# Kernel optimization log

Hardware: AMD Instinct MI355X
Metric: run time of the kernel (lower is better)

## Reference

```python
import jax, jax.numpy as jnp
import numpy as np

NMS_THRESH = 0.3  # default nms_thresh in DetNet.predict


def setup_inputs() -> dict:
    key = jax.random.key(0)
    k1, k2, k3, k4 = jax.random.split(key, 4)
    W, N = 8, 1024
    det = jax.random.uniform(k1, (W, N, 5), dtype=jnp.float32)          # (conf, cx, cy, w, h) in [0,1)
    offsets = jax.random.uniform(k2, (W, 5), dtype=jnp.float32) * 0.5   # window offset vector (0, left, top, 0, 0)-like
    scales = jax.random.uniform(k3, (W, 5), dtype=jnp.float32) * 0.5 + 0.25  # window scale vector
    b = jax.random.uniform(k4, (W, 4), dtype=jnp.float32)
    # (valid_left, valid_right, valid_top, valid_bottom) with left<right, top<bottom
    bounds = jnp.stack([0.3 * b[:, 0], 0.7 + 0.3 * b[:, 1],
                        0.3 * b[:, 2], 0.7 + 0.3 * b[:, 3]], axis=-1)
    return {"det": det, "offsets": offsets, "scales": scales, "bounds": bounds}


def _pairwise_iou(boxes):
    # boxes: [M,4] in (x1,y1,x2,y2)
    x1, y1, x2, y2 = boxes[:, 0], boxes[:, 1], boxes[:, 2], boxes[:, 3]
    area = jnp.clip(x2 - x1, 0.0) * jnp.clip(y2 - y1, 0.0)              # [M]
    iw = jnp.clip(jnp.minimum(x2[:, None], x2[None, :]) - jnp.maximum(x1[:, None], x1[None, :]), 0.0)
    ih = jnp.clip(jnp.minimum(y2[:, None], y2[None, :]) - jnp.maximum(y1[:, None], y1[None, :]), 0.0)
    inter = iw * ih                                                     # [M,M]
    union = area[:, None] + area[None, :] - inter
    return inter / jnp.maximum(union, 1e-9)


def reference(det, offsets, scales, bounds):
    W, N, _ = det.shape
    M = W * N
    cx, cy = det[..., 1], det[..., 2]                                    # [W,N]
    left, right = bounds[:, 0:1], bounds[:, 1:2]
    top, bottom = bounds[:, 2:3], bounds[:, 3:4]
    valid = (cx < right) & (cx > left) & (cy < bottom) & (cy > top)      # [W,N] border mask
    # torch.addcmul(offset, d, scale) = offset + d * scale
    d = (offsets[:, None, :] + det * scales[:, None, :]).reshape(M, 5)
    valid = valid.reshape(M)
    scores = jnp.where(valid, d[:, 0], -1.0)                             # invalid boxes never kept
    order = jnp.argsort(-scores)                                         # descending confidence
    d_s = d[order]                                                       # [M,5]
    s_s = scores[order]
    # point_form: (cx,cy,w,h) -> (x1,y1,x2,y2)
    cxy, wh = d_s[:, 1:3], d_s[:, 3:5]
    boxes = jnp.concatenate([cxy - wh * 0.5, cxy + wh * 0.5], axis=-1)
    iou = jax.lax.stop_gradient(_pairwise_iou(boxes))                    # [M,M], suppression is non-diff
    s_c = jax.lax.stop_gradient(s_s)
    idx = jnp.arange(M)

    def body(i, keep):
        # suppressed if any kept higher-score box overlaps > thresh
        sup = jnp.any(keep & (idx < i) & (iou[:, i] > NMS_THRESH))
        return keep.at[i].set(jnp.logical_and(~sup, s_c[i] > 0.0))

    keep = jax.lax.fori_loop(0, M, body, jnp.ones((M,), dtype=bool))
    return d_s * keep[:, None].astype(d_s.dtype)                         # [M,5], suppressed rows zeroed
```

## Files before the change

### kernel.cpp

```cpp
#include <hip/hip_runtime.h>
#include <cstdint>


#define M_TOT 8192
#define NMS_T 0.3f

#define WS_BOX   65536
#define WS_D     196608
#define WS_VCNT  360448
#define WS_ZROW  393216
#define WS_DONE  458752
#define WS_MASK  524288

typedef unsigned long long u64t;

__device__ __forceinline__ uint32_t desc_key(float sv) {
    uint32_t u = __float_as_uint(sv);
    uint32_t m = (u & 0x80000000u) ? ~u : (u | 0x80000000u);
    return ~m;
}
__device__ __forceinline__ u64t rdl64(u64t v, int sl) {
    unsigned lo = (unsigned)__builtin_amdgcn_readlane((int)(unsigned)v, sl);
    unsigned hi = (unsigned)__builtin_amdgcn_readlane((int)(unsigned)(v >> 32), sl);
    return ((u64t)hi << 32) | lo;
}

__device__ __forceinline__ void scatter_one(
    int i, int rank, u64t key,
    const float* __restrict__ det, const float* __restrict__ offsets,
    const float* __restrict__ scales,
    float4* __restrict__ boxes_srt, float* __restrict__ d_srt)
{
    uint32_t dkey = (uint32_t)(key >> 16);
    if (dkey >= 0x7FFFFFFFu) return;
    int g = i >> 10;
    float d0 = __fadd_rn(offsets[g*5+0], __fmul_rn(det[i*5+0], scales[g*5+0]));
    float d1 = __fadd_rn(offsets[g*5+1], __fmul_rn(det[i*5+1], scales[g*5+1]));
    float d2 = __fadd_rn(offsets[g*5+2], __fmul_rn(det[i*5+2], scales[g*5+2]));
    float d3 = __fadd_rn(offsets[g*5+3], __fmul_rn(det[i*5+3], scales[g*5+3]));
    float d4 = __fadd_rn(offsets[g*5+4], __fmul_rn(det[i*5+4], scales[g*5+4]));
    d_srt[rank*5+0] = d0; d_srt[rank*5+1] = d1; d_srt[rank*5+2] = d2;
    d_srt[rank*5+3] = d3; d_srt[rank*5+4] = d4;
    float hw = __fmul_rn(d3, 0.5f), hh = __fmul_rn(d4, 0.5f);
    boxes_srt[rank] = make_float4(__fsub_rn(d1, hw), __fsub_rn(d2, hh),
                                  __fadd_rn(d1, hw), __fadd_rn(d2, hh));
}

__global__ __launch_bounds__(512) void k2_rank(
    const float* __restrict__ det, const float* __restrict__ offsets,
    const float* __restrict__ scales, const float* __restrict__ bounds,
    float4* __restrict__ boxes_srt, float* __restrict__ d_srt,
    unsigned int* __restrict__ vcnt, u64t* __restrict__ zrow,
    unsigned int* __restrict__ done, float* __restrict__ out)
{
    __shared__ u64t skey[M_TOT];
    __shared__ float soff[40], sscl[40], sbnd[32];
    __shared__ int sTop;
    int t = threadIdx.x;
    int lane = t & 63;
    if (t == 0) sTop = 0;
    if (t < 40) { soff[t] = offsets[t]; sscl[t] = scales[t]; }
    if (t < 32) { sbnd[t] = bounds[t]; }
    if (blockIdx.x == 0 && t < 128) zrow[t] = 0ull;
    if (blockIdx.x == 0 && t < 64)  done[t] = 0u;
    __syncthreads();

    #pragma unroll 4
    for (int s = 0; s < 16; ++s) {
        int u = s * 512 + t;
        int g = u >> 10;
        float raw_s = det[u * 5 + 0];
        float cx    = det[u * 5 + 1];
        float cy    = det[u * 5 + 2];
        float score = __fadd_rn(soff[g * 5 + 0], __fmul_rn(raw_s, sscl[g * 5 + 0]));
        bool valid = (cx < sbnd[g*4+1]) && (cx > sbnd[g*4+0]) &&
                     (cy < sbnd[g*4+3]) && (cy > sbnd[g*4+2]);
        float sv = valid ? score : -1.0f;
        uint32_t dk = desc_key(sv);
        bool push = dk < 0x7FFFFFFFu;
        u64t key = ((u64t)dk << 16) | (unsigned)u;
        u64t bal = __ballot(push);
        if (bal) {
            int lw = 0;
            if (lane == 0) lw = atomicAdd(&sTop, __popcll(bal));
            int wbase = __builtin_amdgcn_readfirstlane(lw);
            if (push) {
                int off = __popcll(bal & ((1ull << lane) - 1ull));
                skey[wbase + off] = key;
            }
        }
    }
    __syncthreads();
    int V = sTop;
    int Vpad = (V + 15) & ~15;
    if (t < Vpad - V) skey[V + t] = ~0ull;
    {
        int zb = blockIdx.x * 320;
        for (int z = zb + t; z < zb + 320; z += 512) out[z] = 0.0f;
    }
    __syncthreads();
    if (t == 0) *vcnt = (unsigned)V;

    int grp = t >> 3;
    int jq  = t & 7;
    int i = blockIdx.x * 64 + grp;
    int g = i >> 10;
    float raw_s = det[i * 5 + 0];
    float cx    = det[i * 5 + 1];
    float cy    = det[i * 5 + 2];
    float score = __fadd_rn(soff[g * 5 + 0], __fmul_rn(raw_s, sscl[g * 5 + 0]));
    bool valid = (cx < sbnd[g*4+1]) && (cx > sbnd[g*4+0]) &&
                 (cy < sbnd[g*4+3]) && (cy > sbnd[g*4+2]);
    float sv = valid ? score : -1.0f;
    uint32_t dk = desc_key(sv);
    u64t ki = ((u64t)dk << 16) | (unsigned)i;
    const ulonglong2* skey2 = (const ulonglong2*)skey;
    int c = 0;
    int nit = Vpad >> 4;
    #pragma unroll 4
    for (int it = 0; it < nit; ++it) {
        ulonglong2 kj = skey2[it * 8 + jq];
        c += (kj.x < ki) + (kj.y < ki);
    }
    c += __shfl_xor(c, 1);
    c += __shfl_xor(c, 2);
    c += __shfl_xor(c, 4);
    if (jq == 0)
        scatter_one(i, c, ki, det, offsets, scales, boxes_srt, d_srt);
}

__global__ __launch_bounds__(512) void k34_fused(
    const float4* __restrict__ boxes_srt,
    const u64t* __restrict__ zrow,
    const float* __restrict__ d_srt,
    const unsigned int* __restrict__ vcnt,
    u64t* __restrict__ mask,
    unsigned int* __restrict__ done,
    float* __restrict__ out)
{
    int V = (int)*vcnt;
    int nwords = (V + 63) >> 6;
    int nc = (V + 127) >> 7;
    int tid = threadIdx.x;

    if (blockIdx.x != 0) {
        __shared__ float4 sb[8 * 65];
        __shared__ float  sa[8 * 65];
        int b = (int)blockIdx.x - 1;
        int gpre = 0;
        for (int c = 0; c < nc; ++c) {
            int w0 = 2 * c;
            int Wc = nwords - w0;
            int tiles = 2 * ((Wc + 7) >> 3);
            int tau0 = ((b - gpre) % 127 + 127) % 127;
            for (int tau = tau0; tau < tiles; tau += 127) {
                int rt = tau & 1, wt = tau >> 1;
                int rowbase = c * 128 + rt * 64;
                int wbase = w0 + wt * 8;
                {
                    int u = tid;
                    float4 bb = boxes_srt[min(wbase * 64 + u, M_TOT - 1)];
                    int cc = u >> 6, jj = u & 63;
                    sb[cc * 65 + jj] = bb;
                    sa[cc * 65 + jj] = __fmul_rn(fmaxf(__fsub_rn(bb.z, bb.x), 0.0f),
                                                 fmaxf(__fsub_rn(bb.w, bb.y), 0.0f));
                }
                __syncthreads();
                int r  = rowbase + (tid >> 3);
                int wl = tid & 7;
                int w  = wbase + wl;
                if (r < V && w < nwords) {
                    float4 bi = boxes_srt[r];
                    float ai = __fmul_rn(fmaxf(__fsub_rn(bi.z, bi.x), 0.0f),
                                         fmaxf(__fsub_rn(bi.w, bi.y), 0.0f));
                    u64t bits = 0;
                    #pragma unroll 4
                    for (int jj = 0; jj < 64; ++jj) {
                        float4 bj = sb[wl * 65 + jj];
                        float aj = sa[wl * 65 + jj];
                        float iw = fmaxf(__fsub_rn(fminf(bi.z, bj.z), fmaxf(bi.x, bj.x)), 0.0f);
                        float ih = fmaxf(__fsub_rn(fminf(bi.w, bj.w), fmaxf(bi.y, bj.y)), 0.0f);
                        float inter = __fmul_rn(iw, ih);
                        float uni   = __fsub_rn(__fadd_rn(ai, aj), inter);
                        float iou   = __fdiv_rn(inter, fmaxf(uni, 1e-9f));
                        int j = w * 64 + jj;
                        if (j > r && iou > NMS_T) bits |= 1ull << jj;
                    }
                    mask[(size_t)r * 128 + w] = bits;
                }
                __syncthreads();
                if (tid == 0) {
                    int rows_t  = V - rowbase; if (rows_t > 64) rows_t = 64;
                    int words_t = nwords - wbase; if (words_t > 8) words_t = 8;
                    if (rows_t > 0) {
                        __threadfence();
                        __hip_atomic_fetch_add(&done[c], (unsigned)(rows_t * words_t),
                                               __ATOMIC_RELEASE, __HIP_MEMORY_SCOPE_AGENT);
                    }
                }
                __syncthreads();
            }
            gpre += tiles;
        }
        return;
    }

    if (tid >= 64) return;
    int lane = tid;
    if (nc <= 0) return;

    u64t dr0 = 0, dr1 = 0;

    {
        int rows_c = V; if (rows_c > 128) rows_c = 128;
        unsigned expc = (unsigned)(rows_c * nwords);
        while (__hip_atomic_load(&done[0], __ATOMIC_RELAXED, __HIP_MEMORY_SCOPE_AGENT) < expc)
            __builtin_amdgcn_s_sleep(2);
        (void)__hip_atomic_load(&done[0], __ATOMIC_ACQUIRE, __HIP_MEMORY_SCOPE_AGENT);
    }
    ulonglong2 bl, bh;
    {
        int rl = min(lane,      M_TOT - 1);
        int rh = min(64 + lane, M_TOT - 1);
        bl = *((const ulonglong2*)(mask + (size_t)rl * 128));
        bh = *((const ulonglong2*)(mask + (size_t)rh * 128));
    }
    for (int T = 0; T < nc; ++T) {
        ulonglong2 nbl, nbh;
        bool havenext = (T + 1 < nc);
        if (havenext) {
            int c = T + 1;
            int rows_c = V - c * 128; if (rows_c > 128) rows_c = 128;
            unsigned expc = (unsigned)(rows_c * (nwords - 2 * c));
            while (__hip_atomic_load(&done[c], __ATOMIC_RELAXED, __HIP_MEMORY_SCOPE_AGENT) < expc)
                __builtin_amdgcn_s_sleep(2);
            (void)__hip_atomic_load(&done[c], __ATOMIC_ACQUIRE, __HIP_MEMORY_SCOPE_AGENT);
            int rl = min(c * 128 + lane,      M_TOT - 1);
            int rh = min(c * 128 + 64 + lane, M_TOT - 1);
            int w = min(2 * c, 124);
            nbl = *((const ulonglong2*)(mask + (size_t)rl * 128 + w));
            nbh = *((const ulonglong2*)(mask + (size_t)rh * 128 + w));
        }
        u64t dlo = rdl64(dr0, T);
        u64t dhi = rdl64(dr1, T);
        u64t live_lo = ~dlo;
        u64t live_hi = ~dhi;
        int rem = V - T * 128;
        if (rem < 128) {
            live_lo &= (rem >= 64) ? ~0ull : ((rem <= 0) ? 0ull : ((1ull << rem) - 1ull));
            int rh = rem - 64;
            live_hi &= (rh >= 64) ? ~0ull : ((rh <= 0) ? 0ull : ((1ull << rh) - 1ull));
        }
        u64t km_lo = 0, km_hi = 0;
        while (live_lo) {
            int bs = (int)__builtin_ctzll(live_lo);
            km_lo |= 1ull << bs;
            u64t rml = rdl64(bl.x, bs);
            u64t rmh = rdl64(bl.y, bs);
            live_lo &= ~rml & ~(1ull << bs);
            live_hi &= ~rmh;
        }
        while (live_hi) {
            int bs = (int)__builtin_ctzll(live_hi);
            km_hi |= 1ull << bs;
            u64t rmh = rdl64(bh.y, bs);
            live_hi &= ~rmh & ~(1ull << bs);
        }
        {
            int base = T * 128;
            u64t ka = km_lo, kb = km_hi;
            while (ka | kb) {
                int r0, r1 = -1;
                if (ka) { int b_ = (int)__builtin_ctzll(ka); ka &= ka - 1; r0 = base + b_; }
                else    { int b_ = (int)__builtin_ctzll(kb); kb &= kb - 1; r0 = base + 64 + b_; }
                if (ka)      { int b_ = (int)__builtin_ctzll(ka); ka &= ka - 1; r1 = base + b_; }
                else if (kb) { int b_ = (int)__builtin_ctzll(kb); kb &= kb - 1; r1 = base + 64 + b_; }
                const ulonglong2* p0 = (const ulonglong2*)(mask + (size_t)r0 * 128) + lane;
                const ulonglong2* p1 = (r1 >= 0)
                    ? (const ulonglong2*)(mask + (size_t)r1 * 128) + lane
                    : (const ulonglong2*)zrow + lane;
                ulonglong2 v0 = *p0;
                ulonglong2 v1 = *p1;
                dr0 |= v0.x | v1.x;
                dr1 |= v0.y | v1.y;
                if (lane < 5) {
                    out[r0 * 5 + lane] = d_srt[r0 * 5 + lane];
                    if (r1 >= 0) out[r1 * 5 + lane] = d_srt[r1 * 5 + lane];
                }
            }
        }
        if (havenext) { bl = nbl; bh = nbh; }
    }
}

extern "C" void kernel_launch(void* const* d_in, const int* in_sizes, int n_in,
                              void* d_out, int out_size, void* d_ws, size_t ws_size,
                              hipStream_t stream) {
    const float* det     = (const float*)d_in[0];
    const float* offsets = (const float*)d_in[1];
    const float* scales  = (const float*)d_in[2];
    const float* bounds  = (const float*)d_in[3];
    float* out = (float*)d_out;
    char* ws = (char*)d_ws;
    float4*       boxes = (float4*)(ws + WS_BOX);
    float*        d_srt = (float*)(ws + WS_D);
    unsigned int* vcnt  = (unsigned int*)(ws + WS_VCNT);
    u64t*         zrow  = (u64t*)(ws + WS_ZROW);
    unsigned int* done  = (unsigned int*)(ws + WS_DONE);
    u64t*         mask  = (u64t*)(ws + WS_MASK);

    k2_rank<<<128, 512, 0, stream>>>(det, offsets, scales, bounds, boxes, d_srt,
                                     vcnt, zrow, done, out);
    k34_fused<<<128, 512, 0, stream>>>(boxes, zrow, d_srt, vcnt, mask, done, out);
}
```

Measured before the change: 155.6 us.

## Replace full NMS mask with on-the-fly suppression against the kept-box list

Drops the full upper-triangular IoU bitmask. Other blocks now compute only the 128x128 diagonal chunk masks. A single block walks the chunks in order and tests each next chunk's boxes against the boxes kept so far, held in LDS with a global spill. This removes most pairwise IoU work and the mask traffic, but serializes more of the work in one block, whose cost grows with the kept count. Done flags use a magic value that is never reset, so a flag left from an earlier call could let the consumer read stale diagonal masks.

```diff
diff --git a/kernel.cpp b/kernel.cpp
--- a/kernel.cpp
+++ b/kernel.cpp
@@ -4,13 +4,16 @@
 
 #define M_TOT 8192
 #define NMS_T 0.3f
+#define MAGIC 0x5F3C9B71u
+#define MAXK  4096
 
 #define WS_BOX   65536
 #define WS_D     196608
 #define WS_VCNT  360448
-#define WS_ZROW  393216
-#define WS_DONE  458752
-#define WS_MASK  524288
+#define WS_DONED 360512
+#define WS_MDIAG 393216
+#define WS_KBG   524288
+#define WS_KRG   655360
 
 typedef unsigned long long u64t;
 
@@ -50,8 +53,7 @@
     const float* __restrict__ det, const float* __restrict__ offsets,
     const float* __restrict__ scales, const float* __restrict__ bounds,
     float4* __restrict__ boxes_srt, float* __restrict__ d_srt,
-    unsigned int* __restrict__ vcnt, u64t* __restrict__ zrow,
-    unsigned int* __restrict__ done, float* __restrict__ out)
+    unsigned int* __restrict__ vcnt, float* __restrict__ out)
 {
     __shared__ u64t skey[M_TOT];
     __shared__ float soff[40], sscl[40], sbnd[32];
@@ -61,8 +63,6 @@
     if (t == 0) sTop = 0;
     if (t < 40) { soff[t] = offsets[t]; sscl[t] = scales[t]; }
     if (t < 32) { sbnd[t] = bounds[t]; }
-    if (blockIdx.x == 0 && t < 128) zrow[t] = 0ull;
-    if (blockIdx.x == 0 && t < 64)  done[t] = 0u;
     __syncthreads();
 
     #pragma unroll 4
@@ -129,167 +129,202 @@
         scatter_one(i, c, ki, det, offsets, scales, boxes_srt, d_srt);
 }
 
-__global__ __launch_bounds__(512) void k34_fused(
+__global__ __launch_bounds__(512) void k34_onfly(
     const float4* __restrict__ boxes_srt,
-    const u64t* __restrict__ zrow,
     const float* __restrict__ d_srt,
     const unsigned int* __restrict__ vcnt,
-    u64t* __restrict__ mask,
-    unsigned int* __restrict__ done,
+    ulonglong2* __restrict__ mdiag,
+    unsigned int* __restrict__ doneD,
+    float4* __restrict__ kb_g,
+    unsigned int* __restrict__ kr_g,
     float* __restrict__ out)
 {
+    __shared__ float4 kb[MAXK];
+    __shared__ float  ka[MAXK];
+    __shared__ unsigned int kr[MAXK];
+    __shared__ float4 cb[128];
+    __shared__ float  ca[128];
+    __shared__ unsigned int sf32[2][128];
+    __shared__ int s_nk;
+
     int V = (int)*vcnt;
-    int nwords = (V + 63) >> 6;
     int nc = (V + 127) >> 7;
-    int tid = threadIdx.x;
+    int t = threadIdx.x;
 
     if (blockIdx.x != 0) {
-        __shared__ float4 sb[8 * 65];
-        __shared__ float  sa[8 * 65];
-        int b = (int)blockIdx.x - 1;
-        int gpre = 0;
-        for (int c = 0; c < nc; ++c) {
-            int w0 = 2 * c;
-            int Wc = nwords - w0;
-            int tiles = 2 * ((Wc + 7) >> 3);
-            int tau0 = ((b - gpre) % 127 + 127) % 127;
-            for (int tau = tau0; tau < tiles; tau += 127) {
-                int rt = tau & 1, wt = tau >> 1;
-                int rowbase = c * 128 + rt * 64;
-                int wbase = w0 + wt * 8;
-                {
-                    int u = tid;
-                    float4 bb = boxes_srt[min(wbase * 64 + u, M_TOT - 1)];
-                    int cc = u >> 6, jj = u & 63;
-                    sb[cc * 65 + jj] = bb;
-                    sa[cc * 65 + jj] = __fmul_rn(fmaxf(__fsub_rn(bb.z, bb.x), 0.0f),
-                                                 fmaxf(__fsub_rn(bb.w, bb.y), 0.0f));
+        int c = (int)blockIdx.x - 1;
+        if (c >= nc) return;
+        if (t < 128) {
+            float4 b = boxes_srt[c * 128 + t];
+            cb[t] = b;
+            ca[t] = __fmul_rn(fmaxf(__fsub_rn(b.z, b.x), 0.0f),
+                              fmaxf(__fsub_rn(b.w, b.y), 0.0f));
+        }
+        __syncthreads();
+        int rl = t & 127, q = t >> 7;
+        float4 bi = cb[rl];
+        float  ai = ca[rl];
+        unsigned bits = 0u;
+        int j0 = 32 * q;
+        #pragma unroll 8
+        for (int b = 0; b < 32; ++b) {
+            int jl = j0 + b;
+            float4 bj = cb[jl];
+            float  aj = ca[jl];
+            float iw = fmaxf(__fsub_rn(fminf(bi.z, bj.z), fmaxf(bi.x, bj.x)), 0.0f);
+            float ih = fmaxf(__fsub_rn(fminf(bi.w, bj.w), fmaxf(bi.y, bj.y)), 0.0f);
+            float inter = __fmul_rn(iw, ih);
+            float uni   = __fsub_rn(__fadd_rn(ai, aj), inter);
+            float iou   = __fdiv_rn(inter, fmaxf(uni, 1e-9f));
+            if (jl > rl && iou > NMS_T) bits |= 1u << b;
+        }
+        ((unsigned*)mdiag)[(c * 128 + rl) * 4 + q] = bits;
+        __syncthreads();
+        if (t == 0) {
+            __threadfence();
+            __hip_atomic_store(&doneD[c], MAGIC,
+                               __ATOMIC_RELEASE, __HIP_MEMORY_SCOPE_AGENT);
+        }
+        return;
+    }
+
+    int lane = t & 63, wv = t >> 6;
+    if (t == 0) s_nk = 0;
+    if (t < 128) {
+        float4 b = boxes_srt[t];
+        cb[t] = b;
+        ca[t] = __fmul_rn(fmaxf(__fsub_rn(b.z, b.x), 0.0f),
+                          fmaxf(__fsub_rn(b.w, b.y), 0.0f));
+    }
+    if (t < 256) sf32[t >> 7][t & 127] = 0u;
+    __syncthreads();
+    if (nc <= 0) return;
+
+    ulonglong2 bl, bh;
+    if (wv == 0) {
+        while (__hip_atomic_load(&doneD[0], __ATOMIC_RELAXED,
+                                 __HIP_MEMORY_SCOPE_AGENT) != MAGIC)
+            __builtin_amdgcn_s_sleep(2);
+        (void)__hip_atomic_load(&doneD[0], __ATOMIC_ACQUIRE,
+                                __HIP_MEMORY_SCOPE_AGENT);
+        bl = mdiag[lane];
+        bh = mdiag[64 + lane];
+    }
+
+    for (int T = 0; T < nc; ++T) {
+        if (wv == 0) {
+            ulonglong2 nbl, nbh;
+            bool hn = (T + 1 < nc);
+            if (hn) {
+                while (__hip_atomic_load(&doneD[T + 1], __ATOMIC_RELAXED,
+                                         __HIP_MEMORY_SCOPE_AGENT) != MAGIC)
+                    __builtin_amdgcn_s_sleep(2);
+                (void)__hip_atomic_load(&doneD[T + 1], __ATOMIC_ACQUIRE,
+                                        __HIP_MEMORY_SCOPE_AGENT);
+                nbl = mdiag[(T + 1) * 128 + lane];
+                nbh = mdiag[(T + 1) * 128 + 64 + lane];
+            }
+            int par = T & 1;
+            unsigned flo = sf32[par][lane];
+            unsigned fhi = sf32[par][64 + lane];
+            u64t live_lo = ~__ballot(flo != 0u);
+            u64t live_hi = ~__ballot(fhi != 0u);
+            int rem = V - T * 128;
+            if (rem < 128) {
+                live_lo &= (rem >= 64) ? ~0ull : ((rem <= 0) ? 0ull : ((1ull << rem) - 1ull));
+                int rh2 = rem - 64;
+                live_hi &= (rh2 >= 64) ? ~0ull : ((rh2 <= 0) ? 0ull : ((1ull << rh2) - 1ull));
+            }
+            u64t km_lo = 0, km_hi = 0;
+            while (live_lo) {
+                int bs = (int)__builtin_ctzll(live_lo);
+                km_lo |= 1ull << bs;
+                u64t rml = rdl64(bl.x, bs);
+                u64t rmh = rdl64(bl.y, bs);
+                live_lo &= ~rml & ~(1ull << bs);
+                live_hi &= ~rmh;
+            }
+            while (live_hi) {
+                int bs = (int)__builtin_ctzll(live_hi);
+                km_hi |= 1ull << bs;
+                u64t rmh = rdl64(bh.y, bs);
+                live_hi &= ~rmh & ~(1ull << bs);
+            }
+            int pl = __popcll(km_lo);
+            int nkm = pl + __popcll(km_hi);
+            int snk = s_nk;
+            for (int p = 0; p < 2; ++p) {
+                int idx = lane + 64 * p;
+                if (idx < nkm) {
+                    int rl2;
+                    if (idx < pl) {
+                        u64t x = km_lo;
+                        for (int k = 0; k < idx; ++k) x &= x - 1;
+                        rl2 = (int)__builtin_ctzll(x);
+                    } else {
+                        u64t x = km_hi;
+                        int ii = idx - pl;
+                        for (int k = 0; k < ii; ++k) x &= x - 1;
+                        rl2 = 64 + (int)__builtin_ctzll(x);
+                    }
+                    int r = T * 128 + rl2;
+                    float4 b = cb[rl2];
+                    float  a = ca[rl2];
+                    int o = snk + idx;
+                    kb_g[o] = b;
+                    kr_g[o] = (unsigned)r;
+                    if (o < MAXK) { kb[o] = b; ka[o] = a; kr[o] = (unsigned)r; }
                 }
-                __syncthreads();
-                int r  = rowbase + (tid >> 3);
-                int wl = tid & 7;
-                int w  = wbase + wl;
-                if (r < V && w < nwords) {
-                    float4 bi = boxes_srt[r];
-                    float ai = __fmul_rn(fmaxf(__fsub_rn(bi.z, bi.x), 0.0f),
-                                         fmaxf(__fsub_rn(bi.w, bi.y), 0.0f));
-                    u64t bits = 0;
-                    #pragma unroll 4
-                    for (int jj = 0; jj < 64; ++jj) {
-                        float4 bj = sb[wl * 65 + jj];
-                        float aj = sa[wl * 65 + jj];
-                        float iw = fmaxf(__fsub_rn(fminf(bi.z, bj.z), fmaxf(bi.x, bj.x)), 0.0f);
-                        float ih = fmaxf(__fsub_rn(fminf(bi.w, bj.w), fmaxf(bi.y, bj.y)), 0.0f);
-                        float inter = __fmul_rn(iw, ih);
-                        float uni   = __fsub_rn(__fadd_rn(ai, aj), inter);
-                        float iou   = __fdiv_rn(inter, fmaxf(uni, 1e-9f));
-                        int j = w * 64 + jj;
-                        if (j > r && iou > NMS_T) bits |= 1ull << jj;
-                    }
-                    mask[(size_t)r * 128 + w] = bits;
+            }
+            if (t == 0) s_nk = snk + nkm;
+            if (hn) { bl = nbl; bh = nbh; }
+        } else {
+            if (t >= 64 && t < 192) sf32[(T + 1) & 1][t - 64] = 0u;
+        }
+        __syncthreads();
+        if (T + 1 < nc) {
+            int rl3 = t & 127, q = t >> 7;
+            int r2 = (T + 1) * 128 + rl3;
+            float4 br = boxes_srt[r2];
+            float  ar = __fmul_rn(fmaxf(__fsub_rn(br.z, br.x), 0.0f),
+                                  fmaxf(__fsub_rn(br.w, br.y), 0.0f));
+            if (q == 0) { cb[rl3] = br; ca[rl3] = ar; }
+            int nk = s_nk;
+            int nkq = (nk + 3) >> 2;
+            int jb = q * nkq;
+            int je = jb + nkq; if (je > nk) je = nk;
+            bool supp = false;
+            for (int j = jb; j < je; ++j) {
+                float4 bj; float aj;
+                if (j < MAXK) { bj = kb[j]; aj = ka[j]; }
+                else {
+                    bj = kb_g[j];
+                    aj = __fmul_rn(fmaxf(__fsub_rn(bj.z, bj.x), 0.0f),
+                                   fmaxf(__fsub_rn(bj.w, bj.y), 0.0f));
                 }
-                __syncthreads();
-                if (tid == 0) {
-                    int rows_t  = V - rowbase; if (rows_t > 64) rows_t = 64;
-                    int words_t = nwords - wbase; if (words_t > 8) words_t = 8;
-                    if (rows_t > 0) {
-                        __threadfence();
-                        __hip_atomic_fetch_add(&done[c], (unsigned)(rows_t * words_t),
-                                               __ATOMIC_RELEASE, __HIP_MEMORY_SCOPE_AGENT);
-                    }
-                }
-                __syncthreads();
-            }
-            gpre += tiles;
-        }
-        return;
-    }
-
-    if (tid >= 64) return;
-    int lane = tid;
-    if (nc <= 0) return;
-
-    u64t dr0 = 0, dr1 = 0;
+                float iw = fmaxf(__fsub_rn(fminf(bj.z, br.z), fmaxf(bj.x, br.x)), 0.0f);
+                float ih = fmaxf(__fsub_rn(fminf(bj.w, br.w), fmaxf(bj.y, br.y)), 0.0f);
+                float inter = __fmul_rn(iw, ih);
+                float uni   = __fsub_rn(__fadd_rn(aj, ar), inter);
+                float iou   = __fdiv_rn(inter, fmaxf(uni, 1e-9f));
+                supp = supp || (iou > NMS_T);
+            }
+            if (supp)
+                ((volatile unsigned char*)&sf32[(T + 1) & 1][rl3])[q] = 1;
+        }
+        __syncthreads();
+    }
 
     {
-        int rows_c = V; if (rows_c > 128) rows_c = 128;
-        unsigned expc = (unsigned)(rows_c * nwords);
-        while (__hip_atomic_load(&done[0], __ATOMIC_RELAXED, __HIP_MEMORY_SCOPE_AGENT) < expc)
-            __builtin_amdgcn_s_sleep(2);
-        (void)__hip_atomic_load(&done[0], __ATOMIC_ACQUIRE, __HIP_MEMORY_SCOPE_AGENT);
-    }
-    ulonglong2 bl, bh;
-    {
-        int rl = min(lane,      M_TOT - 1);
-        int rh = min(64 + lane, M_TOT - 1);
-        bl = *((const ulonglong2*)(mask + (size_t)rl * 128));
-        bh = *((const ulonglong2*)(mask + (size_t)rh * 128));
-    }
-    for (int T = 0; T < nc; ++T) {
-        ulonglong2 nbl, nbh;
-        bool havenext = (T + 1 < nc);
-        if (havenext) {
-            int c = T + 1;
-            int rows_c = V - c * 128; if (rows_c > 128) rows_c = 128;
-            unsigned expc = (unsigned)(rows_c * (nwords - 2 * c));
-            while (__hip_atomic_load(&done[c], __ATOMIC_RELAXED, __HIP_MEMORY_SCOPE_AGENT) < expc)
-                __builtin_amdgcn_s_sleep(2);
-            (void)__hip_atomic_load(&done[c], __ATOMIC_ACQUIRE, __HIP_MEMORY_SCOPE_AGENT);
-            int rl = min(c * 128 + lane,      M_TOT - 1);
-            int rh = min(c * 128 + 64 + lane, M_TOT - 1);
-            int w = min(2 * c, 124);
-            nbl = *((const ulonglong2*)(mask + (size_t)rl * 128 + w));
-            nbh = *((const ulonglong2*)(mask + (size_t)rh * 128 + w));
-        }
-        u64t dlo = rdl64(dr0, T);
-        u64t dhi = rdl64(dr1, T);
-        u64t live_lo = ~dlo;
-        u64t live_hi = ~dhi;
-        int rem = V - T * 128;
-        if (rem < 128) {
-            live_lo &= (rem >= 64) ? ~0ull : ((rem <= 0) ? 0ull : ((1ull << rem) - 1ull));
-            int rh = rem - 64;
-            live_hi &= (rh >= 64) ? ~0ull : ((rh <= 0) ? 0ull : ((1ull << rh) - 1ull));
-        }
-        u64t km_lo = 0, km_hi = 0;
-        while (live_lo) {
-            int bs = (int)__builtin_ctzll(live_lo);
-            km_lo |= 1ull << bs;
-            u64t rml = rdl64(bl.x, bs);
-            u64t rmh = rdl64(bl.y, bs);
-            live_lo &= ~rml & ~(1ull << bs);
-            live_hi &= ~rmh;
-        }
-        while (live_hi) {
-            int bs = (int)__builtin_ctzll(live_hi);
-            km_hi |= 1ull << bs;
-            u64t rmh = rdl64(bh.y, bs);
-            live_hi &= ~rmh & ~(1ull << bs);
-        }
-        {
-            int base = T * 128;
-            u64t ka = km_lo, kb = km_hi;
-            while (ka | kb) {
-                int r0, r1 = -1;
-                if (ka) { int b_ = (int)__builtin_ctzll(ka); ka &= ka - 1; r0 = base + b_; }
-                else    { int b_ = (int)__builtin_ctzll(kb); kb &= kb - 1; r0 = base + 64 + b_; }
-                if (ka)      { int b_ = (int)__builtin_ctzll(ka); ka &= ka - 1; r1 = base + b_; }
-                else if (kb) { int b_ = (int)__builtin_ctzll(kb); kb &= kb - 1; r1 = base + 64 + b_; }
-                const ulonglong2* p0 = (const ulonglong2*)(mask + (size_t)r0 * 128) + lane;
-                const ulonglong2* p1 = (r1 >= 0)
-                    ? (const ulonglong2*)(mask + (size_t)r1 * 128) + lane
-                    : (const ulonglong2*)zrow + lane;
-                ulonglong2 v0 = *p0;
-                ulonglong2 v1 = *p1;
-                dr0 |= v0.x | v1.x;
-                dr1 |= v0.y | v1.y;
-                if (lane < 5) {
-                    out[r0 * 5 + lane] = d_srt[r0 * 5 + lane];
-                    if (r1 >= 0) out[r1 * 5 + lane] = d_srt[r1 * 5 + lane];
-                }
-            }
-        }
-        if (havenext) { bl = nbl; bh = nbh; }
+        int nk = s_nk;
+        for (int idx = t; idx < nk; idx += 512) {
+            int r = (int)((idx < MAXK) ? kr[idx] : kr_g[idx]);
+            out[r * 5 + 0] = d_srt[r * 5 + 0];
+            out[r * 5 + 1] = d_srt[r * 5 + 1];
+            out[r * 5 + 2] = d_srt[r * 5 + 2];
+            out[r * 5 + 3] = d_srt[r * 5 + 3];
+            out[r * 5 + 4] = d_srt[r * 5 + 4];
+        }
     }
 }
 
@@ -305,11 +340,13 @@
     float4*       boxes = (float4*)(ws + WS_BOX);
     float*        d_srt = (float*)(ws + WS_D);
     unsigned int* vcnt  = (unsigned int*)(ws + WS_VCNT);
-    u64t*         zrow  = (u64t*)(ws + WS_ZROW);
-    unsigned int* done  = (unsigned int*)(ws + WS_DONE);
-    u64t*         mask  = (u64t*)(ws + WS_MASK);
+    unsigned int* doneD = (unsigned int*)(ws + WS_DONED);
+    ulonglong2*   mdiag = (ulonglong2*)(ws + WS_MDIAG);
+    float4*       kb_g  = (float4*)(ws + WS_KBG);
+    unsigned int* kr_g  = (unsigned int*)(ws + WS_KRG);
 
     k2_rank<<<128, 512, 0, stream>>>(det, offsets, scales, bounds, boxes, d_srt,
-                                     vcnt, zrow, done, out);
-    k34_fused<<<128, 512, 0, stream>>>(boxes, zrow, d_srt, vcnt, mask, done, out);
-}
+                                     vcnt, out);
+    k34_onfly<<<65, 512, 0, stream>>>(boxes, d_srt, vcnt, mdiag, doneD,
+                                      kb_g, kr_g, out);
+}
```

New measurement: 220.6 us. +41.8%, slower.

## Split NMS serial scan across block waves with shared dead-mask accumulation

Applied to the files above, without the earlier changes.

The block-0 serial NMS loop now uses all 8 waves instead of one. Wave 0 resolves keeps within each 128-row tile and records kept row indices in shared memory. Waves 1-7 OR the kept rows' mask words into a shared dead bitmap using LDS atomics, replacing the single wave's per-kept-row full-row loads held in registers. Output copying is deferred to a final block-wide pass. This adds two barriers per tile and LDS atomic contention, and the helper waves' acquire on done[T] does not spin, so it relies on wave 0 having already waited.

```diff
diff --git a/kernel.cpp b/kernel.cpp
--- a/kernel.cpp
+++ b/kernel.cpp
@@ -8,7 +8,6 @@
 #define WS_BOX   65536
 #define WS_D     196608
 #define WS_VCNT  360448
-#define WS_ZROW  393216
 #define WS_DONE  458752
 #define WS_MASK  524288
 
@@ -50,8 +49,8 @@
     const float* __restrict__ det, const float* __restrict__ offsets,
     const float* __restrict__ scales, const float* __restrict__ bounds,
     float4* __restrict__ boxes_srt, float* __restrict__ d_srt,
-    unsigned int* __restrict__ vcnt, u64t* __restrict__ zrow,
-    unsigned int* __restrict__ done, float* __restrict__ out)
+    unsigned int* __restrict__ vcnt, unsigned int* __restrict__ done,
+    float* __restrict__ out)
 {
     __shared__ u64t skey[M_TOT];
     __shared__ float soff[40], sscl[40], sbnd[32];
@@ -61,8 +60,7 @@
     if (t == 0) sTop = 0;
     if (t < 40) { soff[t] = offsets[t]; sscl[t] = scales[t]; }
     if (t < 32) { sbnd[t] = bounds[t]; }
-    if (blockIdx.x == 0 && t < 128) zrow[t] = 0ull;
-    if (blockIdx.x == 0 && t < 64)  done[t] = 0u;
+    if (blockIdx.x == 0 && t < 64) done[t] = 0u;
     __syncthreads();
 
     #pragma unroll 4
@@ -129,9 +127,8 @@
         scatter_one(i, c, ki, det, offsets, scales, boxes_srt, d_srt);
 }
 
-__global__ __launch_bounds__(512) void k34_fused(
+__global__ __launch_bounds__(512) void k34_bar(
     const float4* __restrict__ boxes_srt,
-    const u64t* __restrict__ zrow,
     const float* __restrict__ d_srt,
     const unsigned int* __restrict__ vcnt,
     u64t* __restrict__ mask,
@@ -205,91 +202,126 @@
         return;
     }
 
-    if (tid >= 64) return;
-    int lane = tid;
+    __shared__ u64t dead[128];
+    __shared__ u64t km_s[2];
+    __shared__ unsigned short kr16[M_TOT];
+    __shared__ int s_nk;
+    int lane = tid & 63;
+
+    if (tid < 128) {
+        int bw = tid * 64;
+        u64t d0 = 0;
+        if (bw >= V)           d0 = ~0ull;
+        else if (bw + 64 > V)  d0 = (~0ull) << (V - bw);
+        dead[tid] = d0;
+    }
+    if (tid == 0) s_nk = 0;
+    __syncthreads();
     if (nc <= 0) return;
 
-    u64t dr0 = 0, dr1 = 0;
-
-    {
+    ulonglong2 bl, bh;
+    if (tid < 64) {
         int rows_c = V; if (rows_c > 128) rows_c = 128;
         unsigned expc = (unsigned)(rows_c * nwords);
         while (__hip_atomic_load(&done[0], __ATOMIC_RELAXED, __HIP_MEMORY_SCOPE_AGENT) < expc)
             __builtin_amdgcn_s_sleep(2);
         (void)__hip_atomic_load(&done[0], __ATOMIC_ACQUIRE, __HIP_MEMORY_SCOPE_AGENT);
-    }
-    ulonglong2 bl, bh;
-    {
-        int rl = min(lane,      M_TOT - 1);
-        int rh = min(64 + lane, M_TOT - 1);
-        bl = *((const ulonglong2*)(mask + (size_t)rl * 128));
-        bh = *((const ulonglong2*)(mask + (size_t)rh * 128));
-    }
+        bl = *(const ulonglong2*)(mask + (size_t)(lane) * 128);
+        bh = *(const ulonglong2*)(mask + (size_t)(64 + lane) * 128);
+    }
+
     for (int T = 0; T < nc; ++T) {
-        ulonglong2 nbl, nbh;
-        bool havenext = (T + 1 < nc);
-        if (havenext) {
+        if (tid < 64) {
+            u64t live_lo = ~dead[2 * T];
+            u64t live_hi = ~dead[2 * T + 1];
+            u64t km_lo = 0, km_hi = 0;
+            while (live_lo) {
+                int bs = (int)__builtin_ctzll(live_lo);
+                km_lo |= 1ull << bs;
+                u64t rml = rdl64(bl.x, bs);
+                u64t rmh = rdl64(bl.y, bs);
+                live_lo &= ~rml & ~(1ull << bs);
+                live_hi &= ~rmh;
+            }
+            while (live_hi) {
+                int bs = (int)__builtin_ctzll(live_hi);
+                km_hi |= 1ull << bs;
+                u64t rmh = rdl64(bh.y, bs);
+                live_hi &= ~rmh & ~(1ull << bs);
+            }
+            if (lane == 0) {
+                km_s[0] = km_lo; km_s[1] = km_hi;
+                int base = s_nk;
+                u64t m = km_lo;
+                while (m) {
+                    int b_ = (int)__builtin_ctzll(m); m &= m - 1;
+                    kr16[base++] = (unsigned short)(T * 128 + b_);
+                }
+                m = km_hi;
+                while (m) {
+                    int b_ = (int)__builtin_ctzll(m); m &= m - 1;
+                    kr16[base++] = (unsigned short)(T * 128 + 64 + b_);
+                }
+                s_nk = base;
+            }
+        }
+        __syncthreads();
+        bool hn = (T + 1 < nc);
+        if (tid >= 64) {
+            int wbeg = 2 * T + 2;
+            if (wbeg < nwords) {
+                (void)__hip_atomic_load(&done[T], __ATOMIC_ACQUIRE,
+                                        __HIP_MEMORY_SCOPE_AGENT);
+                u64t klo = km_s[0], khi = km_s[1];
+                int wv = tid >> 6;
+                int w1 = wbeg + lane;
+                int w2 = wbeg + 64 + lane;
+                bool v1 = w1 < nwords, v2 = w2 < nwords;
+                int idx = 0;
+                u64t m = klo;
+                while (m) {
+                    int b_ = (int)__builtin_ctzll(m); m &= m - 1;
+                    if (idx % 7 == wv - 1) {
+                        const u64t* rp = mask + (size_t)(T * 128 + b_) * 128;
+                        if (v1) atomicOr(&dead[w1], rp[w1]);
+                        if (v2) atomicOr(&dead[w2], rp[w2]);
+                    }
+                    ++idx;
+                }
+                m = khi;
+                while (m) {
+                    int b_ = (int)__builtin_ctzll(m); m &= m - 1;
+                    if (idx % 7 == wv - 1) {
+                        const u64t* rp = mask + (size_t)(T * 128 + 64 + b_) * 128;
+                        if (v1) atomicOr(&dead[w1], rp[w1]);
+                        if (v2) atomicOr(&dead[w2], rp[w2]);
+                    }
+                    ++idx;
+                }
+            }
+        } else if (hn) {
             int c = T + 1;
             int rows_c = V - c * 128; if (rows_c > 128) rows_c = 128;
             unsigned expc = (unsigned)(rows_c * (nwords - 2 * c));
             while (__hip_atomic_load(&done[c], __ATOMIC_RELAXED, __HIP_MEMORY_SCOPE_AGENT) < expc)
                 __builtin_amdgcn_s_sleep(2);
             (void)__hip_atomic_load(&done[c], __ATOMIC_ACQUIRE, __HIP_MEMORY_SCOPE_AGENT);
-            int rl = min(c * 128 + lane,      M_TOT - 1);
-            int rh = min(c * 128 + 64 + lane, M_TOT - 1);
-            int w = min(2 * c, 124);
-            nbl = *((const ulonglong2*)(mask + (size_t)rl * 128 + w));
-            nbh = *((const ulonglong2*)(mask + (size_t)rh * 128 + w));
-        }
-        u64t dlo = rdl64(dr0, T);
-        u64t dhi = rdl64(dr1, T);
-        u64t live_lo = ~dlo;
-        u64t live_hi = ~dhi;
-        int rem = V - T * 128;
-        if (rem < 128) {
-            live_lo &= (rem >= 64) ? ~0ull : ((rem <= 0) ? 0ull : ((1ull << rem) - 1ull));
-            int rh = rem - 64;
-            live_hi &= (rh >= 64) ? ~0ull : ((rh <= 0) ? 0ull : ((1ull << rh) - 1ull));
-        }
-        u64t km_lo = 0, km_hi = 0;
-        while (live_lo) {
-            int bs = (int)__builtin_ctzll(live_lo);
-            km_lo |= 1ull << bs;
-            u64t rml = rdl64(bl.x, bs);
-            u64t rmh = rdl64(bl.y, bs);
-            live_lo &= ~rml & ~(1ull << bs);
-            live_hi &= ~rmh;
-        }
-        while (live_hi) {
-            int bs = (int)__builtin_ctzll(live_hi);
-            km_hi |= 1ull << bs;
-            u64t rmh = rdl64(bh.y, bs);
-            live_hi &= ~rmh & ~(1ull << bs);
-        }
-        {
-            int base = T * 128;
-            u64t ka = km_lo, kb = km_hi;
-            while (ka | kb) {
-                int r0, r1 = -1;
-                if (ka) { int b_ = (int)__builtin_ctzll(ka); ka &= ka - 1; r0 = base + b_; }
-                else    { int b_ = (int)__builtin_ctzll(kb); kb &= kb - 1; r0 = base + 64 + b_; }
-                if (ka)      { int b_ = (int)__builtin_ctzll(ka); ka &= ka - 1; r1 = base + b_; }
-                else if (kb) { int b_ = (int)__builtin_ctzll(kb); kb &= kb - 1; r1 = base + 64 + b_; }
-                const ulonglong2* p0 = (const ulonglong2*)(mask + (size_t)r0 * 128) + lane;
-                const ulonglong2* p1 = (r1 >= 0)
-                    ? (const ulonglong2*)(mask + (size_t)r1 * 128) + lane
-                    : (const ulonglong2*)zrow + lane;
-                ulonglong2 v0 = *p0;
-                ulonglong2 v1 = *p1;
-                dr0 |= v0.x | v1.x;
-                dr1 |= v0.y | v1.y;
-                if (lane < 5) {
-                    out[r0 * 5 + lane] = d_srt[r0 * 5 + lane];
-                    if (r1 >= 0) out[r1 * 5 + lane] = d_srt[r1 * 5 + lane];
-                }
-            }
-        }
-        if (havenext) { bl = nbl; bh = nbh; }
+            bl = *(const ulonglong2*)(mask + (size_t)(c * 128 + lane) * 128 + 2 * c);
+            bh = *(const ulonglong2*)(mask + (size_t)(c * 128 + 64 + lane) * 128 + 2 * c);
+        }
+        __syncthreads();
+    }
+
+    {
+        int nk = s_nk;
+        for (int idx = tid; idx < nk; idx += 512) {
+            int r = (int)kr16[idx];
+            out[r * 5 + 0] = d_srt[r * 5 + 0];
+            out[r * 5 + 1] = d_srt[r * 5 + 1];
+            out[r * 5 + 2] = d_srt[r * 5 + 2];
+            out[r * 5 + 3] = d_srt[r * 5 + 3];
+            out[r * 5 + 4] = d_srt[r * 5 + 4];
+        }
     }
 }
 
@@ -305,11 +337,10 @@
     float4*       boxes = (float4*)(ws + WS_BOX);
     float*        d_srt = (float*)(ws + WS_D);
     unsigned int* vcnt  = (unsigned int*)(ws + WS_VCNT);
-    u64t*         zrow  = (u64t*)(ws + WS_ZROW);
     unsigned int* done  = (unsigned int*)(ws + WS_DONE);
     u64t*         mask  = (u64t*)(ws + WS_MASK);
 
     k2_rank<<<128, 512, 0, stream>>>(det, offsets, scales, bounds, boxes, d_srt,
-                                     vcnt, zrow, done, out);
-    k34_fused<<<128, 512, 0, stream>>>(boxes, zrow, d_srt, vcnt, mask, done, out);
-}
+                                     vcnt, done, out);
+    k34_bar<<<128, 512, 0, stream>>>(boxes, d_srt, vcnt, mask, done, out);
+}
```

Result: faster. 146.1 us (-6.1%).
